# Optimization experiments

Measured on AMD Instinct MI355X. Metric: run time of the kernel, lower is better.

## Reference

```python
import jax, jax.numpy as jnp
import numpy as np

B, C, H, W = 4, 64, 128, 128
Q = 65536
OUT_SIZE = 256  # output image side -> cell = 2/OUT_SIZE
HIDDEN = 256
D_IN = C + 2 + 2  # feat + rel_coord + rel_cell


def setup_inputs() -> dict:
    key = jax.random.key(0)
    ks = jax.random.split(key, 8)
    feat = jax.random.normal(ks[0], (B, C, H, W), dtype=jnp.float32)
    coord = jax.random.uniform(ks[1], (B, Q, 2), dtype=jnp.float32, minval=-1.0, maxval=1.0)
    cell = jnp.full((B, Q, 2), 2.0 / OUT_SIZE, dtype=jnp.float32)

    def lin(k, din, dout):
        return jax.random.normal(k, (din, dout), dtype=jnp.float32) * (1.0 / np.sqrt(din))

    w0 = lin(ks[2], D_IN, HIDDEN)
    w1 = lin(ks[3], HIDDEN, HIDDEN)
    w2 = lin(ks[4], HIDDEN, HIDDEN)
    w3 = lin(ks[5], HIDDEN, HIDDEN)
    w4 = lin(ks[6], HIDDEN, 3)
    z = lambda d: jnp.zeros((d,), dtype=jnp.float32)
    return {"feat": feat, "coord": coord, "cell": cell,
            "w0": w0, "b0": z(HIDDEN), "w1": w1, "b1": z(HIDDEN),
            "w2": w2, "b2": z(HIDDEN), "w3": w3, "b3": z(HIDDEN),
            "w4": w4, "b4": z(3)}


def _liif(feat, coord, cell, ws, bs):
    b, c, h, w = feat.shape
    eps = 1e-6
    rx, ry = 1.0 / h, 1.0 / w  # 2/h/2, 2/w/2
    # local ensemble shifts, loop order vx outer, vy inner: (-1,-1),(-1,1),(1,-1),(1,1)
    shifts = jnp.array([[-rx, -ry], [-rx, ry], [rx, -ry], [rx, ry]], dtype=feat.dtype) + eps
    feat_flat = feat.reshape(b, c, h * w)
    cell_scale = jnp.array([h, w], dtype=feat.dtype)
    rel_cell = cell * cell_scale  # same for all branches

    def branch(shift):
        cshift = jnp.clip(coord + shift, -1.0 + eps, 1.0 - eps)
        # nearest grid_sample, align_corners=False: idx = floor((x+1)*size/2), clamped
        iy = jnp.clip(jnp.floor((cshift[..., 0] + 1.0) * (h * 0.5)), 0.0, h - 1.0).astype(jnp.int32)
        ix = jnp.clip(jnp.floor((cshift[..., 1] + 1.0) * (w * 0.5)), 0.0, w - 1.0).astype(jnp.int32)
        idx = iy * w + ix  # [B, Q]
        q_feat = jnp.take_along_axis(feat_flat, idx[:, None, :], axis=2)  # [B, C, Q]
        q_feat = q_feat.transpose(0, 2, 1)  # [B, Q, C]
        # feat_coord at the gathered pixel (make_coord values)
        qc0 = -1.0 + (2.0 * iy.astype(feat.dtype) + 1.0) / h
        qc1 = -1.0 + (2.0 * ix.astype(feat.dtype) + 1.0) / w
        rel0 = (coord[..., 0] - qc0) * h
        rel1 = (coord[..., 1] - qc1) * w
        inp = jnp.concatenate([q_feat, rel0[..., None], rel1[..., None], rel_cell], axis=-1)
        x = inp
        for wi, bi in zip(ws[:-1], bs[:-1]):
            x = jax.nn.relu(x @ wi + bi)
        pred = x @ ws[-1] + bs[-1]  # [B, Q, 3]
        area = jnp.abs(rel0 * rel1) + 1e-9  # [B, Q]
        return pred, area

    preds, areas = jax.vmap(branch)(shifts)  # [4,B,Q,3], [4,B,Q]
    tot = areas.sum(axis=0)
    # diagonal weight swap: 0<->3, 1<->2  == reverse
    wgt = areas[::-1] / tot
    return (preds * wgt[..., None]).sum(axis=0)  # [B, Q, 3]


def reference(feat, coord, cell, w0, b0, w1, b1, w2, b2, w3, b3, w4, b4):
    ws = [w0, w1, w2, w3, w4]
    bs = [b0, b1, b2, b3, b4]
    return _liif(feat, coord, cell, ws, bs)
```

## Files before the change

### kernel.cpp

```cpp
#include <hip/hip_runtime.h>
#include <cstdint>

typedef __bf16 bf16x8 __attribute__((ext_vector_type(8)));
typedef float f32x4 __attribute__((ext_vector_type(4)));
typedef float f32x16 __attribute__((ext_vector_type(16)));
typedef unsigned int u32x4 __attribute__((ext_vector_type(4)));
typedef unsigned int u32x2 __attribute__((ext_vector_type(2)));
typedef unsigned short u16;
typedef unsigned int u32;

#define HH 128
#define WW 128
#define CC 64
#define QQ 65536
#define BB 4

#define RS 264

#define L0_OFF 0
#define L1_OFF 20480
#define L2_OFF 86016
#define L3_OFF 151552
#define W4_OFF 217088
#define FEATT_BYTE_OFF 524288u

#define LBAR()                                            \
    do {                                                  \
        asm volatile("s_waitcnt lgkmcnt(0)" ::: "memory");\
        __builtin_amdgcn_s_barrier();                     \
        asm volatile("" ::: "memory");                    \
    } while (0)

__global__ void pack_weights(const float* __restrict__ w0,
                             const float* __restrict__ w1,
                             const float* __restrict__ w2,
                             const float* __restrict__ w3,
                             const float* __restrict__ w4,
                             u16* __restrict__ ws_us) {
    int bid = blockIdx.x;
    int lane = threadIdx.x;
    int dst, kbase, n, Ksrc, Ncols;
    const float* w;
    if (bid < 424) {
        int tile, off;
        if (bid < 40)       { tile = bid;       off = L0_OFF; w = w0; Ksrc = 68;  }
        else if (bid < 168) { tile = bid - 40;  off = L1_OFF; w = w1; Ksrc = 256; }
        else if (bid < 296) { tile = bid - 168; off = L2_OFF; w = w2; Ksrc = 256; }
        else                { tile = bid - 296; off = L3_OFF; w = w3; Ksrc = 256; }
        int nt = tile & 7, ks = tile >> 3;
        n = nt * 32 + (lane & 31);
        kbase = ks * 16 + (lane >> 5) * 8;
        Ncols = 256;
        dst = off + tile * 512 + lane * 8;
    } else {
        int kt = bid - 424;
        n = lane & 15;
        kbase = kt * 32 + (lane >> 4) * 8;
        w = w4; Ksrc = 256; Ncols = 3;
        dst = W4_OFF + kt * 512 + lane * 8;
    }
    unsigned int d[4];
    for (int i = 0; i < 4; ++i) {
        unsigned int lo, hi;
        {
            int k = kbase + 2 * i;
            float x = (k < Ksrc && n < Ncols) ? w[k * Ncols + n] : 0.0f;
            __bf16 hb = (__bf16)x;
            lo = (unsigned int)__builtin_bit_cast(u16, hb);
        }
        {
            int k = kbase + 2 * i + 1;
            float x = (k < Ksrc && n < Ncols) ? w[k * Ncols + n] : 0.0f;
            __bf16 hb = (__bf16)x;
            hi = (unsigned int)__builtin_bit_cast(u16, hb);
        }
        d[i] = lo | (hi << 16);
    }
    u32x4 pk = { d[0], d[1], d[2], d[3] };
    *reinterpret_cast<u32x4*>(ws_us + dst) = pk;
}

__global__ void prep_featT(const float* __restrict__ feat, u16* __restrict__ featT) {
    __shared__ u16 tile[128 * 66];
    int bid = blockIdx.x;
    int b = bid >> 7, y = bid & 127;
    for (int idx = threadIdx.x; idx < CC * WW; idx += 256) {
        int c = idx >> 7, x = idx & 127;
        float v = feat[(((b * CC + c) * HH + y) * WW) + x];
        __bf16 hb = (__bf16)v;
        tile[x * 66 + c] = __builtin_bit_cast(u16, hb);
    }
    __syncthreads();
    for (int idx = threadIdx.x; idx < 2048; idx += 256) {
        int x = idx >> 4, c4 = (idx & 15) * 4;
        const u16* src = tile + x * 66 + c4;
        u32x2 d;
        d[0] = (unsigned int)src[0] | ((unsigned int)src[1] << 16);
        d[1] = (unsigned int)src[2] | ((unsigned int)src[3] << 16);
        *reinterpret_cast<u32x2*>(featT + ((b * HH + y) * WW + x) * CC + c4) = d;
    }
}

__device__ __forceinline__ void preload6(u32x4 w[6], const u32x4* __restrict__ b,
                                         int v, int kstr) {
    w[0] = b[v];
    w[1] = b[v + 64];
    w[2] = b[v + kstr];
    w[3] = b[v + kstr + 64];
    w[4] = b[v + 2 * kstr];
    w[5] = b[v + 2 * kstr + 64];
}

template <int NKS>
__device__ __forceinline__ void gemm32(u16* buf,
                                       const u32x4* __restrict__ wbase,
                                       const float* __restrict__ bias,
                                       int wave, int lane,
                                       const u32x4 wpre[6],
                                       u32x4 wnxt[6],
                                       const u32x4* __restrict__ wnb,
                                       int vnxt, int nkstr) {
    f32x16 acc[2][4] = {};
    const int l31 = lane & 31;
    const int hi = lane >> 5;
    const int voff = wave * 128 + lane;
    const u16* xb = buf + l31 * RS + hi * 8;
    u16* db = buf + l31 * RS + wave * 64 + hi * 4;

    u32x4 wq[3][2];
    wq[0][0] = wpre[0]; wq[0][1] = wpre[1];
    wq[1][0] = wpre[2]; wq[1][1] = wpre[3];
    wq[2][0] = wpre[4]; wq[2][1] = wpre[5];

    bf16x8 xc[2][4];
#pragma unroll
    for (int st = 0; st < 4; ++st) {
        xc[0][st] = __builtin_bit_cast(bf16x8,
            *reinterpret_cast<const u32x4*>(xb + st * 32 * RS));
        xc[1][st] = __builtin_bit_cast(bf16x8,
            *reinterpret_cast<const u32x4*>(xb + st * 32 * RS + 16));
    }

#pragma unroll
    for (int ks = 0; ks < NKS; ++ks) {
        const int ws = ks % 3;
        const int xs = ks & 1;
#pragma unroll
        for (int st = 0; st < 4; ++st) {
            acc[0][st] = __builtin_amdgcn_mfma_f32_32x32x16_bf16(
                __builtin_bit_cast(bf16x8, wq[ws][0]), xc[xs][st], acc[0][st], 0, 0, 0);
            acc[1][st] = __builtin_amdgcn_mfma_f32_32x32x16_bf16(
                __builtin_bit_cast(bf16x8, wq[ws][1]), xc[xs][st], acc[1][st], 0, 0, 0);
            if (ks + 2 < NKS)
                xc[xs][st] = __builtin_bit_cast(bf16x8,
                    *reinterpret_cast<const u32x4*>(xb + st * 32 * RS + (ks + 2) * 16));
        }
        if (ks + 3 < NKS) {
            const u32x4* wn = wbase + (ks + 3) * 512;
            wq[ws][0] = wn[voff];
            wq[ws][1] = wn[voff + 64];
        }
    }

    wnxt[0] = wnb[vnxt];
    wnxt[1] = wnb[vnxt + 64];
    wnxt[2] = wnb[vnxt + nkstr];
    wnxt[3] = wnb[vnxt + nkstr + 64];
    wnxt[4] = wnb[vnxt + 2 * nkstr];
    wnxt[5] = wnb[vnxt + 2 * nkstr + 64];

    LBAR();

#pragma unroll
    for (int ft = 0; ft < 2; ++ft) {
        const int fb = wave * 64 + ft * 32 + hi * 4;
#pragma unroll
        for (int q4 = 0; q4 < 4; ++q4) {
            f32x4 bv = *reinterpret_cast<const f32x4*>(bias + fb + q4 * 8);
#pragma unroll
            for (int st = 0; st < 4; ++st) {
                float v0 = fmaxf(acc[ft][st][q4 * 4 + 0] + bv[0], 0.0f);
                float v1 = fmaxf(acc[ft][st][q4 * 4 + 1] + bv[1], 0.0f);
                float v2 = fmaxf(acc[ft][st][q4 * 4 + 2] + bv[2], 0.0f);
                float v3 = fmaxf(acc[ft][st][q4 * 4 + 3] + bv[3], 0.0f);
                u32 lo, hi2;
                asm("v_cvt_pk_bf16_f32 %0, %1, %2" : "=v"(lo)  : "v"(v0), "v"(v1));
                asm("v_cvt_pk_bf16_f32 %0, %1, %2" : "=v"(hi2) : "v"(v2), "v"(v3));
                u32x2 d = { lo, hi2 };
                *reinterpret_cast<u32x2*>(db + st * 32 * RS + ft * 32 + q4 * 8) = d;
            }
        }
    }
}

__global__ __launch_bounds__(256, 2) void liif_main(
    const float* __restrict__ coord, const float* __restrict__ cell,
    const float* __restrict__ b0, const float* __restrict__ b1,
    const float* __restrict__ b2, const float* __restrict__ b3,
    const float* __restrict__ b4,
    const u16* __restrict__ wpack, const u16* __restrict__ featT,
    float* __restrict__ out) {
    __shared__ u16 bufA[128 * RS];
    __shared__ float areasLDS[128];

    const int t = threadIdx.x;
    const int wave = t >> 6, lane = t & 63;
    const int row = t >> 1, p = t & 1;

    const int bq = blockIdx.x * 32 + (row >> 2);
    const int v = row & 3;
    const int b = bq >> 16;
    const float c0 = coord[bq * 2 + 0];
    const float c1 = coord[bq * 2 + 1];
    const float rc0 = cell[bq * 2 + 0] * 128.0f;
    const float rc1 = cell[bq * 2 + 1] * 128.0f;
    const float eps = 1e-6f;
    const float sx = ((v & 2) ? 0.0078125f : -0.0078125f) + eps;
    const float sy = ((v & 1) ? 0.0078125f : -0.0078125f) + eps;
    float cs0 = fminf(fmaxf(c0 + sx, -1.0f + eps), 1.0f - eps);
    float cs1 = fminf(fmaxf(c1 + sy, -1.0f + eps), 1.0f - eps);
    float fy = fminf(fmaxf(floorf((cs0 + 1.0f) * 64.0f), 0.0f), 127.0f);
    float fx = fminf(fmaxf(floorf((cs1 + 1.0f) * 64.0f), 0.0f), 127.0f);
    int iy = (int)fy, ix = (int)fx;
    float qc0 = -1.0f + (2.0f * fy + 1.0f) * 0.0078125f;
    float qc1 = -1.0f + (2.0f * fx + 1.0f) * 0.0078125f;
    float rel0 = (c0 - qc0) * 128.0f;
    float rel1 = (c1 - qc1) * 128.0f;
    float area = fabsf(rel0 * rel1) + 1e-9f;

    {
        const u16* fr = featT + (((b * HH + iy) * WW + ix) * CC) + p * 32;
        u32x4 f0 = *reinterpret_cast<const u32x4*>(fr);
        u32x4 f1 = *reinterpret_cast<const u32x4*>(fr + 8);
        u32x4 f2 = *reinterpret_cast<const u32x4*>(fr + 16);
        u32x4 f3 = *reinterpret_cast<const u32x4*>(fr + 24);
        u16* sb = bufA + row * RS;
        *reinterpret_cast<u32x4*>(sb + p * 32) = f0;
        *reinterpret_cast<u32x4*>(sb + p * 32 + 8) = f1;
        *reinterpret_cast<u32x4*>(sb + p * 32 + 16) = f2;
        *reinterpret_cast<u32x4*>(sb + p * 32 + 24) = f3;
        u32x4 e = { 0u, 0u, 0u, 0u };
        u32x4 z = { 0u, 0u, 0u, 0u };
        if (p == 0) {
            __bf16 h0 = (__bf16)rel0, h1 = (__bf16)rel1, h2 = (__bf16)rc0, h3 = (__bf16)rc1;
            e[0] = (u32)__builtin_bit_cast(u16, h0) | ((u32)__builtin_bit_cast(u16, h1) << 16);
            e[1] = (u32)__builtin_bit_cast(u16, h2) | ((u32)__builtin_bit_cast(u16, h3) << 16);
            areasLDS[row] = area;
        }
        *reinterpret_cast<u32x4*>(sb + 64 + p * 16) = e;
        *reinterpret_cast<u32x4*>(sb + 64 + p * 16 + 8) = z;
    }

    const u32x4* wp = reinterpret_cast<const u32x4*>(wpack);
    const u32x4* wp0 = wp + (L0_OFF / 8);
    const u32x4* wp1 = wp + (L1_OFF / 8);
    const u32x4* wp2 = wp + (L2_OFF / 8);
    const u32x4* wp3 = wp + (L3_OFF / 8);
    const u32x4* wp4 = wp + (W4_OFF / 8);
    const int voff = wave * 128 + lane;

    u32x4 wA[6], wB[6];
    preload6(wA, wp0, voff, 512);
    LBAR();
    gemm32<5>(bufA, wp0, b0, wave, lane, wA, wB, wp1, voff, 512);
    LBAR();
    gemm32<16>(bufA, wp1, b1, wave, lane, wB, wA, wp2, voff, 512);
    LBAR();
    gemm32<16>(bufA, wp2, b2, wave, lane, wA, wB, wp3, voff, 512);
    LBAR();
    gemm32<16>(bufA, wp3, b3, wave, lane, wB, wA, wp4, lane, 128);
    u32x4 w4hi[2];
#pragma unroll
    for (int kt = 0; kt < 2; ++kt) w4hi[kt] = wp4[(kt + 6) * 64 + lane];
    LBAR();

    const int l15 = lane & 15;
    const int qd = lane >> 4;
    const u16* xb4 = bufA + (wave * 32 + l15) * RS + qd * 8;
    f32x4 accf[2] = {};
#pragma unroll
    for (int kt = 0; kt < 8; ++kt) {
        bf16x8 a = __builtin_bit_cast(bf16x8, (kt < 6) ? wA[kt] : w4hi[kt - 6]);
        bf16x8 x0 = __builtin_bit_cast(bf16x8,
            *reinterpret_cast<const u32x4*>(xb4 + kt * 32));
        accf[0] = __builtin_amdgcn_mfma_f32_16x16x32_bf16(a, x0, accf[0], 0, 0, 0);
        bf16x8 x1 = __builtin_bit_cast(bf16x8,
            *reinterpret_cast<const u32x4*>(xb4 + 16 * RS + kt * 32));
        accf[1] = __builtin_amdgcn_mfma_f32_16x16x32_bf16(a, x1, accf[1], 0, 0, 0);
    }
#pragma unroll
    for (int stl = 0; stl < 2; ++stl) {
        float a = areasLDS[wave * 32 + stl * 16 + l15];
        float a1 = a + __shfl_xor(a, 1);
        float asum = a1 + __shfl_xor(a1, 2);
        float aopp = __shfl_xor(a, 3);
        float wgt = aopp / asum;
        float o0 = (accf[stl][0] + b4[0]) * wgt;
        float o1 = (accf[stl][1] + b4[1]) * wgt;
        float o2 = (accf[stl][2] + b4[2]) * wgt;
        o0 += __shfl_xor(o0, 1); o0 += __shfl_xor(o0, 2);
        o1 += __shfl_xor(o1, 1); o1 += __shfl_xor(o1, 2);
        o2 += __shfl_xor(o2, 1); o2 += __shfl_xor(o2, 2);
        if (qd == 0 && (l15 & 3) == 0) {
            int obq = blockIdx.x * 32 + wave * 8 + stl * 4 + (l15 >> 2);
            out[obq * 3 + 0] = o0;
            out[obq * 3 + 1] = o1;
            out[obq * 3 + 2] = o2;
        }
    }
}

extern "C" void kernel_launch(void* const* d_in, const int* in_sizes, int n_in,
                              void* d_out, int out_size, void* d_ws, size_t ws_size,
                              hipStream_t stream) {
    const float* feat  = (const float*)d_in[0];
    const float* coord = (const float*)d_in[1];
    const float* cell  = (const float*)d_in[2];
    const float* w0 = (const float*)d_in[3];
    const float* b0 = (const float*)d_in[4];
    const float* w1 = (const float*)d_in[5];
    const float* b1 = (const float*)d_in[6];
    const float* w2 = (const float*)d_in[7];
    const float* b2 = (const float*)d_in[8];
    const float* w3 = (const float*)d_in[9];
    const float* b3 = (const float*)d_in[10];
    const float* w4 = (const float*)d_in[11];
    const float* b4 = (const float*)d_in[12];

    u16* ws_us = (u16*)d_ws;
    u16* featT = (u16*)((char*)d_ws + FEATT_BYTE_OFF);

    hipLaunchKernelGGL(pack_weights, dim3(432), dim3(64), 0, stream,
                       w0, w1, w2, w3, w4, ws_us);
    hipLaunchKernelGGL(prep_featT, dim3(BB * HH), dim3(256), 0, stream, feat, featT);
    hipLaunchKernelGGL(liif_main, dim3((BB * QQ) / 32), dim3(256), 0, stream,
                       coord, cell, b0, b1, b2, b3, b4, ws_us, featT,
                       (float*)d_out);
}
```

Measured before the change: 479.0 us.

## Shrink block tile to 96 samples for three blocks per CU, drop cross-layer weight prefetch

The per-block sample count drops from 128 to 96 (24 queries), which shrinks LDS use and the accumulator arrays so that launch bounds can ask for three blocks per CU instead of two. The cross-layer weight prefetch that carried the next layer's first weight fragments in registers is removed; each GEMM now loads its own first three k-slices at entry. The final 3-output layer is split across waves unevenly (two waves do two tiles) and gets a tail guard for the non-divisible grid. The aim is higher occupancy to hide latency, at the cost of exposing weight-load latency at each layer start and some load imbalance in the last layer.

```diff
diff --git a/kernel.cpp b/kernel.cpp
--- a/kernel.cpp
+++ b/kernel.cpp
@@ -14,6 +14,9 @@
 #define CC 64
 #define QQ 65536
 #define BB 4
+
+#define SAMP 96
+#define QPB 24
 
 #define RS 264
 
@@ -101,26 +104,12 @@
     }
 }
 
-__device__ __forceinline__ void preload6(u32x4 w[6], const u32x4* __restrict__ b,
-                                         int v, int kstr) {
-    w[0] = b[v];
-    w[1] = b[v + 64];
-    w[2] = b[v + kstr];
-    w[3] = b[v + kstr + 64];
-    w[4] = b[v + 2 * kstr];
-    w[5] = b[v + 2 * kstr + 64];
-}
-
 template <int NKS>
 __device__ __forceinline__ void gemm32(u16* buf,
                                        const u32x4* __restrict__ wbase,
                                        const float* __restrict__ bias,
-                                       int wave, int lane,
-                                       const u32x4 wpre[6],
-                                       u32x4 wnxt[6],
-                                       const u32x4* __restrict__ wnb,
-                                       int vnxt, int nkstr) {
-    f32x16 acc[2][4] = {};
+                                       int wave, int lane) {
+    f32x16 acc[2][3] = {};
     const int l31 = lane & 31;
     const int hi = lane >> 5;
     const int voff = wave * 128 + lane;
@@ -128,13 +117,15 @@
     u16* db = buf + l31 * RS + wave * 64 + hi * 4;
 
     u32x4 wq[3][2];
-    wq[0][0] = wpre[0]; wq[0][1] = wpre[1];
-    wq[1][0] = wpre[2]; wq[1][1] = wpre[3];
-    wq[2][0] = wpre[4]; wq[2][1] = wpre[5];
-
-    bf16x8 xc[2][4];
-#pragma unroll
-    for (int st = 0; st < 4; ++st) {
+#pragma unroll
+    for (int i = 0; i < 3; ++i) {
+        wq[i][0] = wbase[i * 512 + voff];
+        wq[i][1] = wbase[i * 512 + voff + 64];
+    }
+
+    bf16x8 xc[2][3];
+#pragma unroll
+    for (int st = 0; st < 3; ++st) {
         xc[0][st] = __builtin_bit_cast(bf16x8,
             *reinterpret_cast<const u32x4*>(xb + st * 32 * RS));
         xc[1][st] = __builtin_bit_cast(bf16x8,
@@ -146,7 +137,7 @@
         const int ws = ks % 3;
         const int xs = ks & 1;
 #pragma unroll
-        for (int st = 0; st < 4; ++st) {
+        for (int st = 0; st < 3; ++st) {
             acc[0][st] = __builtin_amdgcn_mfma_f32_32x32x16_bf16(
                 __builtin_bit_cast(bf16x8, wq[ws][0]), xc[xs][st], acc[0][st], 0, 0, 0);
             acc[1][st] = __builtin_amdgcn_mfma_f32_32x32x16_bf16(
@@ -162,13 +153,6 @@
         }
     }
 
-    wnxt[0] = wnb[vnxt];
-    wnxt[1] = wnb[vnxt + 64];
-    wnxt[2] = wnb[vnxt + nkstr];
-    wnxt[3] = wnb[vnxt + nkstr + 64];
-    wnxt[4] = wnb[vnxt + 2 * nkstr];
-    wnxt[5] = wnb[vnxt + 2 * nkstr + 64];
-
     LBAR();
 
 #pragma unroll
@@ -178,7 +162,7 @@
         for (int q4 = 0; q4 < 4; ++q4) {
             f32x4 bv = *reinterpret_cast<const f32x4*>(bias + fb + q4 * 8);
 #pragma unroll
-            for (int st = 0; st < 4; ++st) {
+            for (int st = 0; st < 3; ++st) {
                 float v0 = fmaxf(acc[ft][st][q4 * 4 + 0] + bv[0], 0.0f);
                 float v1 = fmaxf(acc[ft][st][q4 * 4 + 1] + bv[1], 0.0f);
                 float v2 = fmaxf(acc[ft][st][q4 * 4 + 2] + bv[2], 0.0f);
@@ -193,42 +177,43 @@
     }
 }
 
-__global__ __launch_bounds__(256, 2) void liif_main(
+__global__ __launch_bounds__(256, 3) void liif_main(
     const float* __restrict__ coord, const float* __restrict__ cell,
     const float* __restrict__ b0, const float* __restrict__ b1,
     const float* __restrict__ b2, const float* __restrict__ b3,
     const float* __restrict__ b4,
     const u16* __restrict__ wpack, const u16* __restrict__ featT,
     float* __restrict__ out) {
-    __shared__ u16 bufA[128 * RS];
-    __shared__ float areasLDS[128];
+    __shared__ u16 bufA[SAMP * RS];
+    __shared__ float areasLDS[SAMP];
 
     const int t = threadIdx.x;
     const int wave = t >> 6, lane = t & 63;
-    const int row = t >> 1, p = t & 1;
-
-    const int bq = blockIdx.x * 32 + (row >> 2);
-    const int v = row & 3;
-    const int b = bq >> 16;
-    const float c0 = coord[bq * 2 + 0];
-    const float c1 = coord[bq * 2 + 1];
-    const float rc0 = cell[bq * 2 + 0] * 128.0f;
-    const float rc1 = cell[bq * 2 + 1] * 128.0f;
-    const float eps = 1e-6f;
-    const float sx = ((v & 2) ? 0.0078125f : -0.0078125f) + eps;
-    const float sy = ((v & 1) ? 0.0078125f : -0.0078125f) + eps;
-    float cs0 = fminf(fmaxf(c0 + sx, -1.0f + eps), 1.0f - eps);
-    float cs1 = fminf(fmaxf(c1 + sy, -1.0f + eps), 1.0f - eps);
-    float fy = fminf(fmaxf(floorf((cs0 + 1.0f) * 64.0f), 0.0f), 127.0f);
-    float fx = fminf(fmaxf(floorf((cs1 + 1.0f) * 64.0f), 0.0f), 127.0f);
-    int iy = (int)fy, ix = (int)fx;
-    float qc0 = -1.0f + (2.0f * fy + 1.0f) * 0.0078125f;
-    float qc1 = -1.0f + (2.0f * fx + 1.0f) * 0.0078125f;
-    float rel0 = (c0 - qc0) * 128.0f;
-    float rel1 = (c1 - qc1) * 128.0f;
-    float area = fabsf(rel0 * rel1) + 1e-9f;
-
-    {
+
+    if (t < 2 * SAMP) {
+        const int row = t >> 1, p = t & 1;
+        int bq = blockIdx.x * QPB + (row >> 2);
+        if (bq > BB * QQ - 1) bq = BB * QQ - 1;
+        const int v = row & 3;
+        const int b = bq >> 16;
+        const float c0 = coord[bq * 2 + 0];
+        const float c1 = coord[bq * 2 + 1];
+        const float rc0 = cell[bq * 2 + 0] * 128.0f;
+        const float rc1 = cell[bq * 2 + 1] * 128.0f;
+        const float eps = 1e-6f;
+        const float sx = ((v & 2) ? 0.0078125f : -0.0078125f) + eps;
+        const float sy = ((v & 1) ? 0.0078125f : -0.0078125f) + eps;
+        float cs0 = fminf(fmaxf(c0 + sx, -1.0f + eps), 1.0f - eps);
+        float cs1 = fminf(fmaxf(c1 + sy, -1.0f + eps), 1.0f - eps);
+        float fy = fminf(fmaxf(floorf((cs0 + 1.0f) * 64.0f), 0.0f), 127.0f);
+        float fx = fminf(fmaxf(floorf((cs1 + 1.0f) * 64.0f), 0.0f), 127.0f);
+        int iy = (int)fy, ix = (int)fx;
+        float qc0 = -1.0f + (2.0f * fy + 1.0f) * 0.0078125f;
+        float qc1 = -1.0f + (2.0f * fx + 1.0f) * 0.0078125f;
+        float rel0 = (c0 - qc0) * 128.0f;
+        float rel1 = (c1 - qc1) * 128.0f;
+        float area = fabsf(rel0 * rel1) + 1e-9f;
+
         const u16* fr = featT + (((b * HH + iy) * WW + ix) * CC) + p * 32;
         u32x4 f0 = *reinterpret_cast<const u32x4*>(fr);
         u32x4 f1 = *reinterpret_cast<const u32x4*>(fr + 8);
@@ -257,55 +242,52 @@
     const u32x4* wp2 = wp + (L2_OFF / 8);
     const u32x4* wp3 = wp + (L3_OFF / 8);
     const u32x4* wp4 = wp + (W4_OFF / 8);
-    const int voff = wave * 128 + lane;
-
-    u32x4 wA[6], wB[6];
-    preload6(wA, wp0, voff, 512);
-    LBAR();
-    gemm32<5>(bufA, wp0, b0, wave, lane, wA, wB, wp1, voff, 512);
-    LBAR();
-    gemm32<16>(bufA, wp1, b1, wave, lane, wB, wA, wp2, voff, 512);
-    LBAR();
-    gemm32<16>(bufA, wp2, b2, wave, lane, wA, wB, wp3, voff, 512);
-    LBAR();
-    gemm32<16>(bufA, wp3, b3, wave, lane, wB, wA, wp4, lane, 128);
-    u32x4 w4hi[2];
-#pragma unroll
-    for (int kt = 0; kt < 2; ++kt) w4hi[kt] = wp4[(kt + 6) * 64 + lane];
+
+    LBAR();
+    gemm32<5>(bufA, wp0, b0, wave, lane);
+    LBAR();
+    gemm32<16>(bufA, wp1, b1, wave, lane);
+    LBAR();
+    gemm32<16>(bufA, wp2, b2, wave, lane);
+    LBAR();
+    gemm32<16>(bufA, wp3, b3, wave, lane);
+    u32x4 w4f[8];
+#pragma unroll
+    for (int kt = 0; kt < 8; ++kt) w4f[kt] = wp4[kt * 64 + lane];
     LBAR();
 
     const int l15 = lane & 15;
     const int qd = lane >> 4;
-    const u16* xb4 = bufA + (wave * 32 + l15) * RS + qd * 8;
-    f32x4 accf[2] = {};
-#pragma unroll
-    for (int kt = 0; kt < 8; ++kt) {
-        bf16x8 a = __builtin_bit_cast(bf16x8, (kt < 6) ? wA[kt] : w4hi[kt - 6]);
-        bf16x8 x0 = __builtin_bit_cast(bf16x8,
-            *reinterpret_cast<const u32x4*>(xb4 + kt * 32));
-        accf[0] = __builtin_amdgcn_mfma_f32_16x16x32_bf16(a, x0, accf[0], 0, 0, 0);
-        bf16x8 x1 = __builtin_bit_cast(bf16x8,
-            *reinterpret_cast<const u32x4*>(xb4 + 16 * RS + kt * 32));
-        accf[1] = __builtin_amdgcn_mfma_f32_16x16x32_bf16(a, x1, accf[1], 0, 0, 0);
-    }
-#pragma unroll
-    for (int stl = 0; stl < 2; ++stl) {
-        float a = areasLDS[wave * 32 + stl * 16 + l15];
+    const int ntile = (wave < 2) ? 2 : 1;
+    for (int stl = 0; stl < ntile; ++stl) {
+        const int tile = wave + stl * 4;
+        const u16* xb4 = bufA + (tile * 16 + l15) * RS + qd * 8;
+        f32x4 accf = {};
+#pragma unroll
+        for (int kt = 0; kt < 8; ++kt) {
+            bf16x8 x = __builtin_bit_cast(bf16x8,
+                *reinterpret_cast<const u32x4*>(xb4 + kt * 32));
+            accf = __builtin_amdgcn_mfma_f32_16x16x32_bf16(
+                __builtin_bit_cast(bf16x8, w4f[kt]), x, accf, 0, 0, 0);
+        }
+        float a = areasLDS[tile * 16 + l15];
         float a1 = a + __shfl_xor(a, 1);
         float asum = a1 + __shfl_xor(a1, 2);
         float aopp = __shfl_xor(a, 3);
         float wgt = aopp / asum;
-        float o0 = (accf[stl][0] + b4[0]) * wgt;
-        float o1 = (accf[stl][1] + b4[1]) * wgt;
-        float o2 = (accf[stl][2] + b4[2]) * wgt;
+        float o0 = (accf[0] + b4[0]) * wgt;
+        float o1 = (accf[1] + b4[1]) * wgt;
+        float o2 = (accf[2] + b4[2]) * wgt;
         o0 += __shfl_xor(o0, 1); o0 += __shfl_xor(o0, 2);
         o1 += __shfl_xor(o1, 1); o1 += __shfl_xor(o1, 2);
         o2 += __shfl_xor(o2, 1); o2 += __shfl_xor(o2, 2);
         if (qd == 0 && (l15 & 3) == 0) {
-            int obq = blockIdx.x * 32 + wave * 8 + stl * 4 + (l15 >> 2);
-            out[obq * 3 + 0] = o0;
-            out[obq * 3 + 1] = o1;
-            out[obq * 3 + 2] = o2;
+            int obq = blockIdx.x * QPB + ((tile * 16 + l15) >> 2);
+            if (obq < BB * QQ) {
+                out[obq * 3 + 0] = o0;
+                out[obq * 3 + 1] = o1;
+                out[obq * 3 + 2] = o2;
+            }
         }
     }
 }
@@ -333,7 +315,7 @@
     hipLaunchKernelGGL(pack_weights, dim3(432), dim3(64), 0, stream,
                        w0, w1, w2, w3, w4, ws_us);
     hipLaunchKernelGGL(prep_featT, dim3(BB * HH), dim3(256), 0, stream, feat, featT);
-    hipLaunchKernelGGL(liif_main, dim3((BB * QQ) / 32), dim3(256), 0, stream,
+    hipLaunchKernelGGL(liif_main, dim3((BB * QQ + QPB - 1) / QPB), dim3(256), 0, stream,
                        coord, cell, b0, b1, b2, b3, b4, ws_us, featT,
                        (float*)d_out);
 }
```

New measurement: 469.1 us, median of 3. 2.1% less time.
